# Performance work log

Measured on AMD Instinct MI355X. Metric: run time of the kernel, lower is better.

Reference implementation:

```python
import jax, jax.numpy as jnp
import numpy as np

B, N, K, H, W = 8, 64, 32, 256, 256


def setup_inputs() -> dict:
    key = jax.random.key(0)
    k1, k2, k3, k4, k5, k6 = jax.random.split(key, 6)
    original = jax.random.normal(k1, (B, 3, H, W), dtype=jnp.float32)
    # loc = (cx, cy, w, h) in normalized coords; keep w,h >= 0.05 so the
    # unnormalized gaussian stays finite.
    cxy = jax.random.uniform(k2, (B, N, 2), dtype=jnp.float32)
    wh = jax.random.uniform(k3, (B, N, 2), dtype=jnp.float32) * 0.45 + 0.05
    loc = jnp.concatenate([cxy, wh], axis=-1)
    masks = jax.random.normal(k4, (B, N, K), dtype=jnp.float32)
    proto = jax.random.normal(k5, (B, H, W, K), dtype=jnp.float32)
    conf = jax.random.uniform(k6, (B, N), dtype=jnp.float32)
    return {"original": original, "loc": loc, "masks": masks,
            "proto": proto, "conf": conf}


def _unnormal_gaussian(loc, h, w):
    # Unnormalized 2D axis-aligned gaussian per prior, evaluated on a
    # half-pixel normalized grid. loc: [B, N, 4] = (cx, cy, sx, sy).
    ys = (jnp.arange(h, dtype=loc.dtype) + 0.5) / h  # [H]
    xs = (jnp.arange(w, dtype=loc.dtype) + 0.5) / w  # [W]
    cx = loc[..., 0][:, :, None, None]
    cy = loc[..., 1][:, :, None, None]
    sx = loc[..., 2][:, :, None, None]
    sy = loc[..., 3][:, :, None, None]
    dy = (ys[None, None, :, None] - cy) / sy  # [B,N,H,1]
    dx = (xs[None, None, None, :] - cx) / sx  # [B,N,1,W]
    return jnp.exp(-0.5 * (dx * dx + dy * dy))  # [B,N,H,W]


def reference(original, loc, masks, proto, conf):
    b, c, h, w = original.shape
    gauss = _unnormal_gaussian(loc, h, w)  # [B,N,H,W]
    # lincomb: sigmoid(proto @ mask_coeffs^T) -> assembled instance masks
    assembled = jax.nn.sigmoid(jnp.einsum('bhwk,bnk->bnhw', proto, masks))
    attention = assembled * gauss                      # [B,N,H,W]
    mask_conf = attention * conf[:, :, None, None]     # einsum 'abcd,ab->abcd'
    denom = jnp.sum(mask_conf, axis=1, keepdims=True) + 1e-5
    final_conf = 1.0 - jnp.sum(mask_conf * mask_conf / denom, axis=1)  # [B,H,W]
    # F.interpolate(..., resizeShape, 'bilinear'): proto res == resizeShape,
    # so this is an identity bilinear resize (half-pixel convention).
    resized_conf = jax.image.resize(final_conf, (b, h, w), method='bilinear')
    total_conf = jnp.sum(resized_conf, axis=0)                        # [H,W]
    weighted_mean = jnp.einsum('bchw,bhw->chw', original, resized_conf)
    squared_diff = (original - weighted_mean) ** 2                    # [B,C,H,W]
    weighted_diff = squared_diff * resized_conf[:, None]  # 'abcd,acd->abcd'
    weighted_variance = weighted_diff / total_conf
    return jnp.sum(weighted_variance)
```

## Files before the change

### kernel.cpp

```cpp
#include <hip/hip_runtime.h>
#include <hip/hip_bf16.h>

#define NPIX 65536
#define NB 8
#define NN 64
#define KK 32
#define LOG2E 1.4426950408889634f

typedef __attribute__((ext_vector_type(4))) float f32x4;
typedef __attribute__((ext_vector_type(8))) short bf16x8;

__device__ __forceinline__ float rcpf(float x) { return __builtin_amdgcn_rcpf(x); }
__device__ __forceinline__ float exp2_fast(float x) { float r; asm("v_exp_f32 %0, %1" : "=v"(r) : "v"(x)); return r; }
__device__ __forceinline__ float log2_fast(float x) { float r; asm("v_log_f32 %0, %1" : "=v"(r) : "v"(x)); return r; }
__device__ __forceinline__ short f2bf(float x) {
    union { __hip_bfloat16 b; short s; } u; u.b = __float2bfloat16(x); return u.s;
}

__global__ __launch_bounds__(256) void k_phase1(
    const float* __restrict__ loc,
    const float* __restrict__ masks,
    const float* __restrict__ proto,
    const float* __restrict__ conf,
    float* __restrict__ fcb)
{
    __shared__ float4 sprm[NN];

    const int b    = blockIdx.x >> 8;
    const int row  = blockIdx.x & 255;
    const int tid  = threadIdx.x;
    const int lane = tid & 63;
    const int wave = tid >> 6;
    const int nl   = lane & 15;
    const int kg   = lane >> 4;

    const float inv = 1.0f / 256.0f;
    const float fy  = (row + 0.5f) * inv;

    if (tid < NN) {
        float4 L = ((const float4*)loc)[b * NN + tid];
        float isx = rcpf(L.z), isy = rcpf(L.w);
        float gx = -0.72134752f * isx * isx;
        float gy = -0.72134752f * isy * isy;
        float dy = fy - L.y;
        float ey = fmaf(dy * dy, gy, log2_fast(conf[b * NN + tid]));
        sprm[tid] = make_float4(L.x, gx, ey, 0.f);
    }
    __syncthreads();

    int mi[4], ni[4];
    {
        bf16x8 Ap, Bp;
#pragma unroll
        for (int j = 0; j < 8; ++j) { Ap[j] = 0; Bp[j] = 0; }
        if (kg == 0) {
            Ap[0] = f2bf((float)nl);
            Ap[1] = f2bf(1.0f);
            Bp[0] = f2bf(1.0f);
            Bp[1] = f2bf((float)(16 * nl));
        }
        f32x4 z = {0.f, 0.f, 0.f, 0.f};
        f32x4 d = __builtin_amdgcn_mfma_f32_16x16x32_bf16(Ap, Bp, z, 0, 0, 0);
#pragma unroll
        for (int r = 0; r < 4; ++r) {
            int v = (int)(d[r] + 0.5f);
            mi[r] = v & 15;
            ni[r] = (v >> 4) & 15;
        }
    }
    const int ni0 = ni[0];

    bf16x8 Mf[4];
#pragma unroll
    for (int t = 0; t < 4; ++t) {
        const float* mp = masks + ((size_t)b * NN + 16 * t + nl) * KK + kg * 8;
        float4 u0 = *(const float4*)mp;
        float4 u1 = *(const float4*)(mp + 4);
        bf16x8 v;
        v[0] = f2bf(u0.x * -LOG2E); v[1] = f2bf(u0.y * -LOG2E);
        v[2] = f2bf(u0.z * -LOG2E); v[3] = f2bf(u0.w * -LOG2E);
        v[4] = f2bf(u1.x * -LOG2E); v[5] = f2bf(u1.y * -LOG2E);
        v[6] = f2bf(u1.z * -LOG2E); v[7] = f2bf(u1.w * -LOG2E);
        Mf[t] = v;
    }

    float Pcx[4][4], Pgx[4][4], Pey[4][4];
#pragma unroll
    for (int t = 0; t < 4; ++t)
#pragma unroll
        for (int r = 0; r < 4; ++r) {
            float4 P = sprm[16 * t + mi[r]];
            Pcx[t][r] = P.x; Pgx[t][r] = P.y; Pey[t][r] = P.z;
        }

#define EVALT(ACC, T)                                                      \
    {                                                                      \
        _Pragma("unroll") for (int r = 0; r < 4; ++r) {                    \
            float dx = fx - Pcx[T][r];                                     \
            float e  = fmaf(dx * dx, Pgx[T][r], Pey[T][r]);                \
            float a  = exp2_fast(e) * rcpf(1.0f + exp2_fast(ACC[r]));      \
            S1 += a; S2 = fmaf(a, a, S2);                                  \
        }                                                                  \
    }

    const size_t prow = (size_t)b * NPIX + row * 256;
    for (int i = 0; i < 4; ++i) {
        const int cb = wave * 64 + i * 16;
        const float* pp = proto + (prow + cb + nl) * KK + kg * 8;
        float4 a0 = *(const float4*)pp;
        float4 a1 = *(const float4*)(pp + 4);
        bf16x8 Pf;
        Pf[0] = f2bf(a0.x); Pf[1] = f2bf(a0.y); Pf[2] = f2bf(a0.z); Pf[3] = f2bf(a0.w);
        Pf[4] = f2bf(a1.x); Pf[5] = f2bf(a1.y); Pf[6] = f2bf(a1.z); Pf[7] = f2bf(a1.w);

        f32x4 z = {0.f, 0.f, 0.f, 0.f};
        f32x4 acc0 = __builtin_amdgcn_mfma_f32_16x16x32_bf16(Mf[0], Pf, z, 0, 0, 0);
        f32x4 acc1 = __builtin_amdgcn_mfma_f32_16x16x32_bf16(Mf[1], Pf, z, 0, 0, 0);
        f32x4 acc2 = __builtin_amdgcn_mfma_f32_16x16x32_bf16(Mf[2], Pf, z, 0, 0, 0);
        f32x4 acc3 = __builtin_amdgcn_mfma_f32_16x16x32_bf16(Mf[3], Pf, z, 0, 0, 0);

        const float fx = (cb + ni0 + 0.5f) * inv;
        float S1 = 0.f, S2 = 0.f;
        EVALT(acc0, 0);
        EVALT(acc1, 1);
        EVALT(acc2, 2);
        EVALT(acc3, 3);

        S1 += __shfl_xor(S1, 16); S1 += __shfl_xor(S1, 32);
        S2 += __shfl_xor(S2, 16); S2 += __shfl_xor(S2, 32);
        if (lane < 16)
            fcb[prow + cb + ni0] = 1.0f - S2 * rcpf(S1 + 1e-5f);
    }
#undef EVALT
}

__global__ __launch_bounds__(256) void k_phase2(
    const float* __restrict__ original,
    const float* __restrict__ fcb,
    float* __restrict__ out)
{
    const int pix = blockIdx.x * 256 + threadIdx.x;

    float f[NB];
    float tot = 0.f;
#pragma unroll
    for (int b = 0; b < NB; ++b) { f[b] = fcb[(size_t)b * NPIX + pix]; tot += f[b]; }

    float part = 0.f;
#pragma unroll
    for (int c = 0; c < 3; ++c) {
        float o[NB];
        float wm = 0.f;
#pragma unroll
        for (int b = 0; b < NB; ++b) {
            o[b] = original[((size_t)(b * 3 + c)) * NPIX + pix];
            wm = fmaf(o[b], f[b], wm);
        }
#pragma unroll
        for (int b = 0; b < NB; ++b) {
            float d = o[b] - wm;
            part = fmaf(d * d, f[b], part);
        }
    }
    part *= rcpf(tot);

#pragma unroll
    for (int off = 32; off > 0; off >>= 1) part += __shfl_down(part, off);
    __shared__ float sred[4];
    if ((threadIdx.x & 63) == 0) sred[threadIdx.x >> 6] = part;
    __syncthreads();
    if (threadIdx.x == 0) atomicAdd(out, sred[0] + sred[1] + sred[2] + sred[3]);
}

__global__ __launch_bounds__(256) void k_fused(
    const float* __restrict__ original, const float* __restrict__ loc,
    const float* __restrict__ masks, const float* __restrict__ proto,
    const float* __restrict__ conf, float* __restrict__ out)
{
    const int pix = blockIdx.x * 256 + threadIdx.x;
    const float inv = 1.0f / 256.0f;
    const float fx = ((pix & 255) + 0.5f) * inv;
    const float fy = ((pix >> 8) + 0.5f) * inv;

    float f[NB];
    for (int b = 0; b < NB; ++b) {
        const float4* p4 = (const float4*)(proto + ((size_t)b * NPIX + pix) * KK);
        const float4* m4 = (const float4*)(masks + (size_t)b * NN * KK);
        const float4* l4 = (const float4*)(loc + (size_t)b * NN * 4);
        const float*  cf = conf + b * NN;
        float S1 = 0.f, S2 = 0.f;
        for (int n = 0; n < NN; ++n) {
            float sa = 0.f;
#pragma unroll
            for (int j = 0; j < 8; ++j) {
                float4 A = p4[j], m = m4[n * 8 + j];
                sa = fmaf(A.w, m.w, fmaf(A.z, m.z, fmaf(A.y, m.y, fmaf(A.x, m.x, sa))));
            }
            const float4 L = l4[n];
            float isx = rcpf(L.z), isy = rcpf(L.w);
            float dx = (fx - L.x) * isx, dy = (fy - L.y) * isy;
            float g = __expf(-0.5f * fmaf(dx, dx, dy * dy));
            float a = g * rcpf(1.0f + __expf(-sa)) * cf[n];
            S1 += a;
            S2 = fmaf(a, a, S2);
        }
        f[b] = 1.0f - S2 * rcpf(S1 + 1e-5f);
    }
    float tot = 0.f;
#pragma unroll
    for (int b = 0; b < NB; ++b) tot += f[b];
    float part = 0.f;
#pragma unroll
    for (int c = 0; c < 3; ++c) {
        float o[NB];
        float wm = 0.f;
#pragma unroll
        for (int b = 0; b < NB; ++b) {
            o[b] = original[((size_t)(b * 3 + c)) * NPIX + pix];
            wm = fmaf(o[b], f[b], wm);
        }
#pragma unroll
        for (int b = 0; b < NB; ++b) {
            float d = o[b] - wm;
            part = fmaf(d * d, f[b], part);
        }
    }
    part *= rcpf(tot);

#pragma unroll
    for (int off = 32; off > 0; off >>= 1) part += __shfl_down(part, off);
    __shared__ float sred[4];
    if ((threadIdx.x & 63) == 0) sred[threadIdx.x >> 6] = part;
    __syncthreads();
    if (threadIdx.x == 0) atomicAdd(out, sred[0] + sred[1] + sred[2] + sred[3]);
}

extern "C" void kernel_launch(void* const* d_in, const int* in_sizes, int n_in,
                              void* d_out, int out_size, void* d_ws, size_t ws_size,
                              hipStream_t stream) {
    const float* original = (const float*)d_in[0];
    const float* loc      = (const float*)d_in[1];
    const float* masks    = (const float*)d_in[2];
    const float* proto    = (const float*)d_in[3];
    const float* conf     = (const float*)d_in[4];
    float* out = (float*)d_out;

    hipMemsetAsync(out, 0, sizeof(float), stream);

    const size_t fc_bytes = (size_t)NB * NPIX * sizeof(float);
    if (ws_size >= fc_bytes) {
        float* fcb = (float*)d_ws;
        k_phase1<<<NB * 256, 256, 0, stream>>>(loc, masks, proto, conf, fcb);
        k_phase2<<<NPIX / 256, 256, 0, stream>>>(original, fcb, out);
    } else {
        k_fused<<<NPIX / 256, 256, 0, stream>>>(original, loc, masks, proto, conf, out);
    }
}
```

Measured before the change: 38.24 us.

## Process two rows per block, prefetch proto loads, and expand gaussian quadratic

Each phase-1 block now handles two image rows (two waves per row), which halves the grid and amortizes the per-block parameter setup and mask loads. Each wave covers 128 pixels in an unrolled loop that software-prefetches the next proto chunk while the current one runs through MFMA and the exp math. The gaussian exponent is precomputed as a quadratic in x, so each term costs two FMAs instead of a subtract, multiply and FMA. This trades higher register pressure and fewer blocks for better load-latency hiding.

```diff
diff --git a/kernel.cpp b/kernel.cpp
--- a/kernel.cpp
+++ b/kernel.cpp
@@ -24,27 +24,33 @@
     const float* __restrict__ conf,
     float* __restrict__ fcb)
 {
-    __shared__ float4 sprm[NN];
-
-    const int b    = blockIdx.x >> 8;
-    const int row  = blockIdx.x & 255;
+    __shared__ float4 sprm[2][NN];
+
+    const int b    = blockIdx.x >> 7;
+    const int rp   = blockIdx.x & 127;
     const int tid  = threadIdx.x;
     const int lane = tid & 63;
     const int wave = tid >> 6;
     const int nl   = lane & 15;
     const int kg   = lane >> 4;
+    const int rw   = wave >> 1;
+    const int half = wave & 1;
+    const int row  = rp * 2 + rw;
 
     const float inv = 1.0f / 256.0f;
-    const float fy  = (row + 0.5f) * inv;
-
-    if (tid < NN) {
-        float4 L = ((const float4*)loc)[b * NN + tid];
+
+    if (tid < 128) {
+        const int rr = tid >> 6, n = tid & 63;
+        float4 L = ((const float4*)loc)[b * NN + n];
         float isx = rcpf(L.z), isy = rcpf(L.w);
         float gx = -0.72134752f * isx * isx;
         float gy = -0.72134752f * isy * isy;
-        float dy = fy - L.y;
-        float ey = fmaf(dy * dy, gy, log2_fast(conf[b * NN + tid]));
-        sprm[tid] = make_float4(L.x, gx, ey, 0.f);
+        float fyr = (rp * 2 + rr + 0.5f) * inv;
+        float dy  = fyr - L.y;
+        float ey  = fmaf(dy * dy, gy, log2_fast(conf[b * NN + n]));
+        float beta  = -2.0f * gx * L.x;
+        float gamma = fmaf(gx * L.x, L.x, ey);
+        sprm[rr][n] = make_float4(gx, beta, gamma, 0.f);
     }
     __syncthreads();
 
@@ -84,34 +90,43 @@
         Mf[t] = v;
     }
 
-    float Pcx[4][4], Pgx[4][4], Pey[4][4];
+    float Pa[4][4], Pb[4][4], Pc[4][4];
 #pragma unroll
     for (int t = 0; t < 4; ++t)
 #pragma unroll
         for (int r = 0; r < 4; ++r) {
-            float4 P = sprm[16 * t + mi[r]];
-            Pcx[t][r] = P.x; Pgx[t][r] = P.y; Pey[t][r] = P.z;
-        }
-
-#define EVALT(ACC, T)                                                      \
-    {                                                                      \
-        _Pragma("unroll") for (int r = 0; r < 4; ++r) {                    \
-            float dx = fx - Pcx[T][r];                                     \
-            float e  = fmaf(dx * dx, Pgx[T][r], Pey[T][r]);                \
-            float a  = exp2_fast(e) * rcpf(1.0f + exp2_fast(ACC[r]));      \
-            S1 += a; S2 = fmaf(a, a, S2);                                  \
-        }                                                                  \
-    }
-
-    const size_t prow = (size_t)b * NPIX + row * 256;
-    for (int i = 0; i < 4; ++i) {
-        const int cb = wave * 64 + i * 16;
-        const float* pp = proto + (prow + cb + nl) * KK + kg * 8;
-        float4 a0 = *(const float4*)pp;
-        float4 a1 = *(const float4*)(pp + 4);
+            float4 P = sprm[rw][16 * t + mi[r]];
+            Pa[t][r] = P.x; Pb[t][r] = P.y; Pc[t][r] = P.z;
+        }
+
+#define EVALT(ACC, T)                                                       \
+    {                                                                       \
+        _Pragma("unroll") for (int r = 0; r < 4; ++r) {                     \
+            float e  = fmaf(fmaf(Pa[T][r], fx, Pb[T][r]), fx, Pc[T][r]);    \
+            float aa = exp2_fast(e) * rcpf(1.0f + exp2_fast(ACC[r]));       \
+            S1 += aa; S2 = fmaf(aa, aa, S2);                                \
+        }                                                                   \
+    }
+
+    const size_t prow = (size_t)b * NPIX + (size_t)row * 256;
+    const int pxb = half * 128;
+    const float* pp0 = proto + (prow + pxb + nl) * KK + kg * 8;
+
+    float4 c0 = *(const float4*)(pp0);
+    float4 c1 = *(const float4*)(pp0 + 4);
+
+#pragma unroll
+    for (int i = 0; i < 8; ++i) {
+        float4 n0, n1;
+        if (i < 7) {
+            const float* np = pp0 + (size_t)(i + 1) * 16 * KK;
+            n0 = *(const float4*)np;
+            n1 = *(const float4*)(np + 4);
+        }
+
         bf16x8 Pf;
-        Pf[0] = f2bf(a0.x); Pf[1] = f2bf(a0.y); Pf[2] = f2bf(a0.z); Pf[3] = f2bf(a0.w);
-        Pf[4] = f2bf(a1.x); Pf[5] = f2bf(a1.y); Pf[6] = f2bf(a1.z); Pf[7] = f2bf(a1.w);
+        Pf[0] = f2bf(c0.x); Pf[1] = f2bf(c0.y); Pf[2] = f2bf(c0.z); Pf[3] = f2bf(c0.w);
+        Pf[4] = f2bf(c1.x); Pf[5] = f2bf(c1.y); Pf[6] = f2bf(c1.z); Pf[7] = f2bf(c1.w);
 
         f32x4 z = {0.f, 0.f, 0.f, 0.f};
         f32x4 acc0 = __builtin_amdgcn_mfma_f32_16x16x32_bf16(Mf[0], Pf, z, 0, 0, 0);
@@ -119,7 +134,7 @@
         f32x4 acc2 = __builtin_amdgcn_mfma_f32_16x16x32_bf16(Mf[2], Pf, z, 0, 0, 0);
         f32x4 acc3 = __builtin_amdgcn_mfma_f32_16x16x32_bf16(Mf[3], Pf, z, 0, 0, 0);
 
-        const float fx = (cb + ni0 + 0.5f) * inv;
+        const float fx = (pxb + i * 16 + ni0 + 0.5f) * inv;
         float S1 = 0.f, S2 = 0.f;
         EVALT(acc0, 0);
         EVALT(acc1, 1);
@@ -129,7 +144,9 @@
         S1 += __shfl_xor(S1, 16); S1 += __shfl_xor(S1, 32);
         S2 += __shfl_xor(S2, 16); S2 += __shfl_xor(S2, 32);
         if (lane < 16)
-            fcb[prow + cb + ni0] = 1.0f - S2 * rcpf(S1 + 1e-5f);
+            fcb[prow + pxb + i * 16 + ni0] = 1.0f - S2 * rcpf(S1 + 1e-5f);
+
+        if (i < 7) { c0 = n0; c1 = n1; }
     }
 #undef EVALT
 }
@@ -250,7 +267,7 @@
     const size_t fc_bytes = (size_t)NB * NPIX * sizeof(float);
     if (ws_size >= fc_bytes) {
         float* fcb = (float*)d_ws;
-        k_phase1<<<NB * 256, 256, 0, stream>>>(loc, masks, proto, conf, fcb);
+        k_phase1<<<NB * 128, 256, 0, stream>>>(loc, masks, proto, conf, fcb);
         k_phase2<<<NPIX / 256, 256, 0, stream>>>(original, fcb, out);
     } else {
         k_fused<<<NPIX / 256, 256, 0, stream>>>(original, loc, masks, proto, conf, out);
```

Measured after the change: 35.56 us. 1.08x faster.
